# Kernel tuning notes

Hardware: AMD Instinct MI355X
Metric: run time of the kernel (lower is better)

The kernel has to match this reference:

```python
import jax, jax.numpy as jnp
import numpy as np

D = 768      # num_hiddens (hardcoded by dense1/dense2/ln in the source)
H = 12       # num_heads
NEG = -1000000.0
EPS = 1e-5


def setup_inputs() -> dict:
    key = jax.random.key(0)
    ks = jax.random.split(key, 14)
    B, Lq, Lk = 8, 1024, 1024
    s = 0.02
    return {
        "queries": jax.random.normal(ks[0], (B, Lq, D), dtype=jnp.float32),
        "keys":    jax.random.normal(ks[1], (B, Lk, D), dtype=jnp.float32),
        "values":  jax.random.normal(ks[2], (B, Lk, D), dtype=jnp.float32),
        # binary padding masks; count_nonzero along axis 1 gives valid lens
        "mask_1": jax.random.randint(ks[3], (B, Lk), 0, 2, dtype=jnp.int32),
        "mask_2": jax.random.randint(ks[4], (B, Lq), 0, 2, dtype=jnp.int32),
        # projection weights stored as [in, out] (torch Linear is y = x @ W.T)
        "Wq": jax.random.normal(ks[5], (D, D), dtype=jnp.float32) * s,
        "Wk": jax.random.normal(ks[6], (D, D), dtype=jnp.float32) * s,
        "Wv": jax.random.normal(ks[7], (D, D), dtype=jnp.float32) * s,
        "Wo": jax.random.normal(ks[8], (D, D), dtype=jnp.float32) * s,
        "d1_w": jax.random.normal(ks[9], (D, D), dtype=jnp.float32) * s,
        "d1_b": jnp.zeros((D,), dtype=jnp.float32),
        "d2_w": jax.random.normal(ks[10], (D, D), dtype=jnp.float32) * s,
        "d2_b": jnp.zeros((D,), dtype=jnp.float32),
        "ln_g": jnp.ones((D,), dtype=jnp.float32),
        "ln_b": jnp.zeros((D,), dtype=jnp.float32),
    }


def _cross_att(queries, keys, values, mask_1, mask_2,
               Wq, Wk, Wv, Wo, d1_w, d1_b, d2_w, d2_b, ln_g, ln_b):
    B, Lq, _ = queries.shape
    Lk = keys.shape[1]
    hd = D // H
    # project + split heads: [B, H, L, hd]
    q = (queries @ Wq).reshape(B, Lq, H, hd).transpose(0, 2, 1, 3)
    k = (keys    @ Wk).reshape(B, Lk, H, hd).transpose(0, 2, 1, 3)
    v = (values  @ Wv).reshape(B, Lk, H, hd).transpose(0, 2, 1, 3)
    scores = jnp.einsum('bhqd,bhkd->bhqk', q, k) / jnp.sqrt(jnp.float32(hd))
    # dual-axis prefix mask from nonzero counts
    vl1 = jnp.sum(mask_1 != 0, axis=1)  # [B], masks key axis
    vl2 = jnp.sum(mask_2 != 0, axis=1)  # [B], masks query axis
    col_ok = jnp.arange(Lk)[None, None, None, :] < vl1[:, None, None, None]
    row_ok = jnp.arange(Lq)[None, None, :, None] < vl2[:, None, None, None]
    scores = jnp.where(col_ok & row_ok, scores, NEG)
    attn = jax.nn.softmax(scores, axis=-1)
    out = jnp.einsum('bhqk,bhkd->bhqd', attn, v)
    out = out.transpose(0, 2, 1, 3).reshape(B, Lq, D)
    mha = out @ Wo
    ffn = jax.nn.relu(mha @ d1_w + d1_b) @ d2_w + d2_b
    x = ffn + mha  # dropout is identity in eval
    mu = jnp.mean(x, axis=-1, keepdims=True)
    var = jnp.mean(jnp.square(x - mu), axis=-1, keepdims=True)
    return (x - mu) / jnp.sqrt(var + EPS) * ln_g + ln_b


def reference(queries, keys, values, mask_1, mask_2,
              Wq, Wk, Wv, Wo, d1_w, d1_b, d2_w, d2_b, ln_g, ln_b):
    return _cross_att(queries, keys, values, mask_1, mask_2,
                      Wq, Wk, Wv, Wo, d1_w, d1_b, d2_w, d2_b, ln_g, ln_b)
```

## Files before the change

kernel.cpp:

```cpp
#include <hip/hip_runtime.h>
#include <hip/hip_bf16.h>
#include <type_traits>

#define DM   768
#define NH   12
#define HD   64
#define BATCH 8
#define SEQ  1024
#define NROWS (BATCH * SEQ)

typedef short bf16x8 __attribute__((ext_vector_type(8)));
typedef float f32x4 __attribute__((ext_vector_type(4)));

__device__ inline unsigned short f2b(float x) {
    union { float f; unsigned int u; } v; v.f = x;
    return (unsigned short)((v.u + 0x8000u) >> 16);
}
__device__ inline unsigned int f2b2(float lo, float hi) {
    union { float f; unsigned int u; } a, b; a.f = lo; b.f = hi;
    return __builtin_amdgcn_perm(b.u + 0x8000u, a.u + 0x8000u, 0x07060302u);
}
__device__ inline float b2f(unsigned short u) {
    union { float f; unsigned int x; } v; v.x = ((unsigned int)u) << 16;
    return v.f;
}

__device__ inline void gld16(const unsigned short* g, unsigned short* l) {
    __builtin_amdgcn_global_load_lds(
        (const __attribute__((address_space(1))) unsigned int*)g,
        (__attribute__((address_space(3))) unsigned int*)l, 16, 0, 0);
}

__device__ __forceinline__ void mm2(const unsigned short* __restrict__ A,
                                    const unsigned short* __restrict__ Wt,
                                    int m0, int n0, int t,
                                    unsigned short (*As)[128][32],
                                    unsigned short (*Ws)[128][32],
                                    f32x4 (&acc)[4][4]) {
    const int w = t >> 6, lane = t & 63;
    const int quad = lane >> 4, l16 = lane & 15;
    const int wm = w & 1, wn = w >> 1;
    const int srow = 16 * w + (lane >> 2);
    const int scol = 8 * ((lane & 3) ^ ((lane >> 3) & 3));
    const int swr = (quad ^ ((l16 >> 1) & 3)) * 8;

#pragma unroll
    for (int i = 0; i < 4; ++i)
#pragma unroll
        for (int j = 0; j < 4; ++j) acc[i][j] = (f32x4){0.f, 0.f, 0.f, 0.f};

#pragma unroll
    for (int j = 0; j < 2; ++j) {
        gld16(&A[(size_t)(m0 + srow + 64 * j) * DM + scol], &As[0][16 * w + 64 * j][0]);
        gld16(&Wt[(size_t)(n0 + srow + 64 * j) * DM + scol], &Ws[0][16 * w + 64 * j][0]);
    }
    __syncthreads();

    for (int k0 = 0; k0 < DM; k0 += 32) {
        const int cur = (k0 >> 5) & 1;
        if (k0 + 32 < DM) {
#pragma unroll
            for (int j = 0; j < 2; ++j) {
                gld16(&A[(size_t)(m0 + srow + 64 * j) * DM + k0 + 32 + scol],
                      &As[cur ^ 1][16 * w + 64 * j][0]);
                gld16(&Wt[(size_t)(n0 + srow + 64 * j) * DM + k0 + 32 + scol],
                      &Ws[cur ^ 1][16 * w + 64 * j][0]);
            }
        }
        bf16x8 av[4], bv[4];
#pragma unroll
        for (int i = 0; i < 4; ++i)
            av[i] = *(const bf16x8*)&As[cur][wm * 64 + 16 * i + l16][swr];
#pragma unroll
        for (int i = 0; i < 4; ++i)
            bv[i] = *(const bf16x8*)&Ws[cur][wn * 64 + 16 * i + l16][swr];
#pragma unroll
        for (int i = 0; i < 4; ++i)
#pragma unroll
            for (int j = 0; j < 4; ++j)
                acc[i][j] = __builtin_amdgcn_mfma_f32_16x16x32_bf16(bv[j], av[i], acc[i][j], 0, 0, 0);
        __syncthreads();
    }
}

__global__ __launch_bounds__(256) void prep_kernel(const float* __restrict__ w0,
                                                   const float* __restrict__ w1,
                                                   const float* __restrict__ w2,
                                                   const float* __restrict__ w3,
                                                   const float* __restrict__ w4,
                                                   const float* __restrict__ w5,
                                                   unsigned short* __restrict__ wt,
                                                   unsigned short* __restrict__ wob,
                                                   const float* __restrict__ qin,
                                                   const float* __restrict__ kin,
                                                   const float* __restrict__ vin,
                                                   unsigned short* __restrict__ oq,
                                                   unsigned short* __restrict__ ok,
                                                   unsigned short* __restrict__ ov) {
    const int z = blockIdx.z;
    const int t = threadIdx.x;

    if (z >= 6) {
        const int linear = (z - 6) * 576 + blockIdx.y * 24 + blockIdx.x;
        const int c0 = linear * 4;
        const int g = c0 / 3072;
        const int r = c0 % 3072;
        const float* src = (g == 0) ? qin : (g == 1) ? kin : vin;
        unsigned short* dst = (g == 0) ? oq : (g == 1) ? ok : ov;
        const size_t i = ((size_t)r * 256 + t) * 8;
        float4 f[8];
#pragma unroll
        for (int c = 0; c < 4; ++c) {
            f[2 * c]     = ((const float4*)(src + i + (size_t)c * 2048))[0];
            f[2 * c + 1] = ((const float4*)(src + i + (size_t)c * 2048))[1];
        }
#pragma unroll
        for (int c = 0; c < 4; ++c) {
            uint4 p;
            p.x = f2b2(f[2 * c].x, f[2 * c].y);
            p.y = f2b2(f[2 * c].z, f[2 * c].w);
            p.z = f2b2(f[2 * c + 1].x, f[2 * c + 1].y);
            p.w = f2b2(f[2 * c + 1].z, f[2 * c + 1].w);
            *(uint4*)(dst + i + (size_t)c * 2048) = p;
        }
        return;
    }

    {
        __shared__ float tile[32][33];
        const float* W = (z == 0) ? w0 : (z == 1) ? w1 : (z == 2) ? w2
                       : (z == 3) ? w3 : (z == 4) ? w4 : w5;
        unsigned short* Wt = wt + (size_t)z * DM * DM;
        const int n0 = blockIdx.x * 32;
        const int k0 = blockIdx.y * 32;
        const int tx = t & 31;
        const int ty = t >> 5;
        float v[4];
#pragma unroll
        for (int r = 0; r < 4; ++r) {
            v[r] = W[(size_t)(k0 + ty + 8 * r) * DM + n0 + tx];
            tile[ty + 8 * r][tx] = v[r];
        }
        if (z == 3) {
#pragma unroll
            for (int r = 0; r < 4; ++r)
                wob[(size_t)(k0 + ty + 8 * r) * DM + n0 + tx] = f2b(v[r]);
        }
        __syncthreads();
#pragma unroll
        for (int r = 0; r < 4; ++r)
            Wt[(size_t)(n0 + ty + 8 * r) * DM + k0 + tx] = f2b(tile[tx][ty + 8 * r]);
    }
}

__global__ __launch_bounds__(256) void qkv_gemm(const unsigned short* __restrict__ aq,
                                                const unsigned short* __restrict__ akk,
                                                const unsigned short* __restrict__ av_,
                                                unsigned short* __restrict__ wt,
                                                const unsigned short* __restrict__ wob,
                                                unsigned short* __restrict__ c0,
                                                unsigned short* __restrict__ c1,
                                                unsigned short* __restrict__ c2,
                                                const int* __restrict__ m1,
                                                const int* __restrict__ m2,
                                                int* __restrict__ lens) {
    __shared__ __align__(16) unsigned short As[2][128][32];
    __shared__ __align__(16) unsigned short Ws[2][128][32];

    const int t = threadIdx.x;
    const size_t WT = (size_t)DM * DM;

    const unsigned short* A;
    const unsigned short* Wop;
    unsigned short* C;
    float cs = 1.0f;
    int m0, n0;

    if (blockIdx.y == 0) {
        if (blockIdx.x >= 52) return;
        if (blockIdx.x >= 36) {
            const int bid = blockIdx.x - 36;
            int* redi = (int*)&As[0][0][0];
            const int b = bid & 7;
            const int* m = (bid < 8) ? m1 : m2;
            int cnt = 0;
            for (int i = t; i < SEQ; i += 256) cnt += (m[b * SEQ + i] != 0) ? 1 : 0;
            redi[t] = cnt;
            __syncthreads();
            for (int off = 128; off > 0; off >>= 1) {
                if (t < off) redi[t] += redi[t + off];
                __syncthreads();
            }
            if (t == 0) lens[bid] = redi[0];
            return;
        }
        A = wt + 4 * WT;
        Wop = wob;
        C = wt + 6 * WT;
        m0 = (blockIdx.x % 6) * 128;
        n0 = (blockIdx.x / 6) * 128;
    } else {
        const int yy = blockIdx.y - 1;
        const int g = yy / 6;
        m0 = blockIdx.x * 128;
        n0 = (yy % 6) * 128;
        A = (g == 0) ? aq : (g == 1) ? akk : av_;
        Wop = wt + (size_t)g * WT;
        C = (g == 0) ? c0 : (g == 1) ? c1 : c2;
        cs = (g == 0) ? 0.18033688f : 1.0f;
    }

    f32x4 acc[4][4];
    mm2(A, Wop, m0, n0, t, As, Ws, acc);

    const int w = t >> 6, lane = t & 63;
    const int quad = lane >> 4, l16 = lane & 15;
    const int wm = w & 1, wn = w >> 1;

#pragma unroll
    for (int i = 0; i < 4; ++i) {
        const int tok = m0 + wm * 64 + 16 * i + l16;
        unsigned short* crow = &C[(size_t)tok * DM + n0 + wn * 64 + quad * 4];
#pragma unroll
        for (int j = 0; j < 4; ++j) {
            uint2 pr;
            pr.x = f2b2(acc[i][j][0] * cs, acc[i][j][1] * cs);
            pr.y = f2b2(acc[i][j][2] * cs, acc[i][j][3] * cs);
            *(uint2*)(crow + 16 * j) = pr;
        }
    }
}

__global__ __launch_bounds__(256) void vpart_kernel(const unsigned short* __restrict__ v,
                                                    float* __restrict__ vp) {
    __shared__ float red[4][64];
    const int t = threadIdx.x;
    const int bh = blockIdx.x;
    const int chunk = blockIdx.y;
    const int b = bh / NH, h = bh % NH;
    const int d = t & 63, rg = t >> 6;
    const unsigned short* base =
        v + (size_t)(b * SEQ + chunk * 128 + rg * 32) * DM + h * HD + d;
    float s = 0.0f;
#pragma unroll 4
    for (int i = 0; i < 32; ++i) s += b2f(base[(size_t)i * DM]);
    red[rg][d] = s;
    __syncthreads();
    if (rg == 0)
        vp[((size_t)bh * 8 + chunk) * 64 + d] = red[0][d] + red[1][d] + red[2][d] + red[3][d];
}

template <typename CT>
__global__ __launch_bounds__(256) void gemm_bf(const unsigned short* __restrict__ A,
                                               const unsigned short* __restrict__ Wt,
                                               CT* __restrict__ C,
                                               const float* __restrict__ bias,
                                               const unsigned short* __restrict__ res,
                                               int relu) {
    __shared__ __align__(16) unsigned short As[2][128][32];
    __shared__ __align__(16) unsigned short Ws[2][128][32];

    const int t = threadIdx.x;
    const int m0 = blockIdx.x * 128;
    const int n0 = blockIdx.y * 128;

    f32x4 acc[4][4];
    mm2(A, Wt, m0, n0, t, As, Ws, acc);

    const int w = t >> 6, lane = t & 63;
    const int quad = lane >> 4, l16 = lane & 15;
    const int wm = w & 1, wn = w >> 1;

#pragma unroll
    for (int i = 0; i < 4; ++i) {
        const int tok = m0 + wm * 64 + 16 * i + l16;
#pragma unroll
        for (int j = 0; j < 4; ++j) {
            const int fb = n0 + wn * 64 + 16 * j + quad * 4;
            float cv0 = acc[i][j][0], cv1 = acc[i][j][1];
            float cv2 = acc[i][j][2], cv3 = acc[i][j][3];
            if (bias) {
                const float4 bb = *(const float4*)&bias[fb];
                cv0 += bb.x; cv1 += bb.y; cv2 += bb.z; cv3 += bb.w;
            }
            if (relu) {
                cv0 = fmaxf(cv0, 0.0f); cv1 = fmaxf(cv1, 0.0f);
                cv2 = fmaxf(cv2, 0.0f); cv3 = fmaxf(cv3, 0.0f);
            }
            if (res) {
                const uint2 rr = *(const uint2*)&res[(size_t)tok * DM + fb];
                cv0 += b2f((unsigned short)(rr.x & 0xffffu));
                cv1 += b2f((unsigned short)(rr.x >> 16));
                cv2 += b2f((unsigned short)(rr.y & 0xffffu));
                cv3 += b2f((unsigned short)(rr.y >> 16));
            }
            if constexpr (std::is_same<CT, float>::value) {
                float4 o4; o4.x = cv0; o4.y = cv1; o4.z = cv2; o4.w = cv3;
                *(float4*)&C[(size_t)tok * DM + fb] = o4;
            } else {
                uint2 pr;
                pr.x = f2b2(cv0, cv1);
                pr.y = f2b2(cv2, cv3);
                *(uint2*)&C[(size_t)tok * DM + fb] = pr;
            }
        }
    }
}

__global__ __launch_bounds__(256) void gemm_mh(const unsigned short* __restrict__ A,
                                               const unsigned short* __restrict__ wt,
                                               unsigned short* __restrict__ cm,
                                               unsigned short* __restrict__ ch,
                                               const float* __restrict__ d1b) {
    __shared__ __align__(16) unsigned short As[2][128][32];
    __shared__ __align__(16) unsigned short Ws[2][128][32];

    const int t = threadIdx.x;
    const int unit = blockIdx.y / 6;
    const unsigned short* Wt = wt + (size_t)(unit ? 6 : 3) * DM * DM;
    unsigned short* C = unit ? ch : cm;
    const int m0 = blockIdx.x * 128;
    const int n0 = (blockIdx.y % 6) * 128;

    f32x4 acc[4][4];
    mm2(A, Wt, m0, n0, t, As, Ws, acc);

    const int w = t >> 6, lane = t & 63;
    const int quad = lane >> 4, l16 = lane & 15;
    const int wm = w & 1, wn = w >> 1;

#pragma unroll
    for (int i = 0; i < 4; ++i) {
        const int tok = m0 + wm * 64 + 16 * i + l16;
#pragma unroll
        for (int j = 0; j < 4; ++j) {
            const int fb = n0 + wn * 64 + 16 * j + quad * 4;
            float cv0 = acc[i][j][0], cv1 = acc[i][j][1];
            float cv2 = acc[i][j][2], cv3 = acc[i][j][3];
            if (unit) {
                const float4 bb = *(const float4*)&d1b[fb];
                cv0 = fmaxf(cv0 + bb.x, 0.0f);
                cv1 = fmaxf(cv1 + bb.y, 0.0f);
                cv2 = fmaxf(cv2 + bb.z, 0.0f);
                cv3 = fmaxf(cv3 + bb.w, 0.0f);
            }
            uint2 pr;
            pr.x = f2b2(cv0, cv1);
            pr.y = f2b2(cv2, cv3);
            *(uint2*)&C[(size_t)tok * DM + fb] = pr;
        }
    }
}

__global__ __launch_bounds__(256) void attn_mfma(const unsigned short* Q,
                                                 const unsigned short* __restrict__ K,
                                                 const unsigned short* __restrict__ V,
                                                 unsigned short* O,
                                                 const int* __restrict__ lens,
                                                 const float* __restrict__ vp) {
    __shared__ __align__(16) unsigned short Ks[64][72];
    __shared__ __align__(16) unsigned short Vt[64][72];
    __shared__ __align__(16) unsigned short Ps[4][16][72];

    const int t = threadIdx.x;
    const int bid = blockIdx.x;
    const int q0 = (bid & 15) * 64;
    const int h = (bid >> 4) % NH;
    const int b = bid / (16 * NH);
    const int vl1 = lens[b];
    const int vl2 = lens[8 + b];
    const int wid = t >> 6;
    const int lane = t & 63;
    const int quad = lane >> 4;
    const int l16 = lane & 15;
    const size_t vpb = (size_t)(b * NH + h) * 8 * 64;

    if (q0 >= vl2 || vl1 == 0) {
        float vm[4];
#pragma unroll
        for (int ct = 0; ct < 4; ++ct) {
            float s = 0.0f;
#pragma unroll
            for (int c = 0; c < 8; ++c) s += vp[vpb + (size_t)c * 64 + 16 * ct + l16];
            vm[ct] = s * (1.0f / 1024.0f);
        }
#pragma unroll
        for (int r = 0; r < 4; ++r) {
            const size_t row = (size_t)(b * SEQ + q0 + 16 * wid + quad * 4 + r);
#pragma unroll
            for (int ct = 0; ct < 4; ++ct)
                O[row * DM + h * HD + 16 * ct + l16] = f2b(vm[ct]);
        }
        return;
    }

    bf16x8 qa0, qa1;
    {
        const unsigned short* qp =
            &Q[(size_t)(b * SEQ + q0 + 16 * wid + l16) * DM + h * HD + quad * 8];
        qa0 = *(const bf16x8*)qp;
        qa1 = *(const bf16x8*)(qp + 32);
    }

    f32x4 o[4];
#pragma unroll
    for (int ct = 0; ct < 4; ++ct) o[ct] = (f32x4){0.f, 0.f, 0.f, 0.f};
    float suml[4];
    bool rbad[4];
#pragma unroll
    for (int r = 0; r < 4; ++r) {
        suml[r] = 0.0f;
        rbad[r] = (q0 + 16 * wid + quad * 4 + r) >= vl2;
    }

    const int nt = (vl1 + 63) >> 6;

    const int kkr = t >> 3;
    const int khc = (t & 7) * 8;
    const unsigned short* kbase = &K[(size_t)(b * SEQ) * DM + h * HD];
    const unsigned short* vbase = &V[(size_t)(b * SEQ) * DM + h * HD];

    uint4 kr0 = *(const uint4*)&kbase[(size_t)kkr * DM + khc];
    uint4 kr1 = *(const uint4*)&kbase[(size_t)(kkr + 32) * DM + khc];
    uint4 vr0 = *(const uint4*)&vbase[(size_t)lane * DM + wid * 16];
    uint4 vr1 = *(const uint4*)&vbase[(size_t)lane * DM + wid * 16 + 8];

    const int k2 = l16 >> 2;

    for (int tile = 0; tile < nt; ++tile) {
        const int c0 = tile * 64;
        *(uint4*)&Ks[kkr][khc] = kr0;
        *(uint4*)&Ks[kkr + 32][khc] = kr1;
        {
            union { uint4 u; unsigned short s[8]; } va, vb;
            va.u = vr0; vb.u = vr1;
#pragma unroll
            for (int j = 0; j < 8; ++j) Vt[wid * 16 + j][lane] = va.s[j];
#pragma unroll
            for (int j = 0; j < 8; ++j) Vt[wid * 16 + 8 + j][lane] = vb.s[j];
        }
        __syncthreads();

        if (tile < nt - 1) {
            const int c1 = c0 + 64;
            kr0 = *(const uint4*)&kbase[(size_t)(c1 + kkr) * DM + khc];
            kr1 = *(const uint4*)&kbase[(size_t)(c1 + kkr + 32) * DM + khc];
            vr0 = *(const uint4*)&vbase[(size_t)(c1 + lane) * DM + wid * 16];
            vr1 = *(const uint4*)&vbase[(size_t)(c1 + lane) * DM + wid * 16 + 8];
        }

        f32x4 s[4];
#pragma unroll
        for (int ct = 0; ct < 4; ++ct) {
            f32x4 acc = (f32x4){0.f, 0.f, 0.f, 0.f};
            bf16x8 b0v = *(const bf16x8*)&Ks[16 * ct + l16][quad * 8];
            bf16x8 b1v = *(const bf16x8*)&Ks[16 * ct + l16][32 + quad * 8];
            acc = __builtin_amdgcn_mfma_f32_16x16x32_bf16(qa0, b0v, acc, 0, 0, 0);
            acc = __builtin_amdgcn_mfma_f32_16x16x32_bf16(qa1, b1v, acc, 0, 0, 0);
            s[ct] = acc;
        }
#pragma unroll
        for (int ct = 0; ct < 4; ++ct) {
            const bool kok = (c0 + 16 * ct + l16) < vl1;
#pragma unroll
            for (int r = 0; r < 4; ++r) {
                float e = __builtin_amdgcn_exp2f(s[ct][r]);
                float p = kok ? e : 0.0f;
                s[ct][r] = p;
                suml[r] += p;
            }
        }
#pragma unroll
        for (int ct = 0; ct < 4; ++ct) {
            const int gidx = 2 * ct + (l16 >> 3);
            const int c = l16 & 7;
            const int gs = (gidx ^ quad) * 8 + c;
#pragma unroll
            for (int r = 0; r < 4; ++r)
                Ps[wid][quad * 4 + r][gs] = f2b(s[ct][r]);
        }
        bf16x8 pa0 = *(const bf16x8*)&Ps[wid][l16][(quad ^ k2) * 8];
        bf16x8 pa1 = *(const bf16x8*)&Ps[wid][l16][((4 + quad) ^ k2) * 8];
#pragma unroll
        for (int ct = 0; ct < 4; ++ct) {
            bf16x8 vb0 = *(const bf16x8*)&Vt[16 * ct + l16][quad * 8];
            bf16x8 vb1 = *(const bf16x8*)&Vt[16 * ct + l16][32 + quad * 8];
            o[ct] = __builtin_amdgcn_mfma_f32_16x16x32_bf16(pa0, vb0, o[ct], 0, 0, 0);
            o[ct] = __builtin_amdgcn_mfma_f32_16x16x32_bf16(pa1, vb1, o[ct], 0, 0, 0);
        }
        __syncthreads();
    }

#pragma unroll
    for (int d = 1; d < 16; d <<= 1) {
#pragma unroll
        for (int r = 0; r < 4; ++r) suml[r] += __shfl_xor(suml[r], d, 64);
    }

    float vm[4];
    if (rbad[0] || rbad[3]) {
#pragma unroll
        for (int ct = 0; ct < 4; ++ct) {
            float s = 0.0f;
#pragma unroll
            for (int c = 0; c < 8; ++c) s += vp[vpb + (size_t)c * 64 + 16 * ct + l16];
            vm[ct] = s * (1.0f / 1024.0f);
        }
    }
#pragma unroll
    for (int r = 0; r < 4; ++r) {
        const float inv = 1.0f / suml[r];
        const size_t row = (size_t)(b * SEQ + q0 + 16 * wid + quad * 4 + r);
#pragma unroll
        for (int ct = 0; ct < 4; ++ct) {
            const float val = rbad[r] ? vm[ct] : o[ct][r] * inv;
            O[row * DM + h * HD + 16 * ct + l16] = f2b(val);
        }
    }
}

__global__ __launch_bounds__(256) void ln_kernel(float* __restrict__ X,
                                                 const float* __restrict__ g,
                                                 const float* __restrict__ bvec) {
    __shared__ float red[256];
    const int row = blockIdx.x;
    const int t = threadIdx.x;
    float* xr = X + (size_t)row * DM;
    float x0 = xr[t];
    float x1 = xr[t + 256];
    float x2 = xr[t + 512];
    red[t] = x0 + x1 + x2;
    __syncthreads();
    for (int off = 128; off > 0; off >>= 1) {
        if (t < off) red[t] += red[t + off];
        __syncthreads();
    }
    float mu = red[0] * (1.0f / 768.0f);
    __syncthreads();
    float d0 = x0 - mu, d1 = x1 - mu, d2 = x2 - mu;
    red[t] = d0 * d0 + d1 * d1 + d2 * d2;
    __syncthreads();
    for (int off = 128; off > 0; off >>= 1) {
        if (t < off) red[t] += red[t + off];
        __syncthreads();
    }
    float rstd = rsqrtf(red[0] * (1.0f / 768.0f) + 1e-5f);
    xr[t]       = d0 * rstd * g[t]       + bvec[t];
    xr[t + 256] = d1 * rstd * g[t + 256] + bvec[t + 256];
    xr[t + 512] = d2 * rstd * g[t + 512] + bvec[t + 512];
}

extern "C" void kernel_launch(void* const* d_in, const int* in_sizes, int n_in,
                              void* d_out, int out_size, void* d_ws, size_t ws_size,
                              hipStream_t stream) {
    const float* queries = (const float*)d_in[0];
    const float* keys    = (const float*)d_in[1];
    const float* values  = (const float*)d_in[2];
    const int* mask1 = (const int*)d_in[3];
    const int* mask2 = (const int*)d_in[4];
    const float* Wq  = (const float*)d_in[5];
    const float* Wk  = (const float*)d_in[6];
    const float* Wv  = (const float*)d_in[7];
    const float* Wo  = (const float*)d_in[8];
    const float* d1w = (const float*)d_in[9];
    const float* d1b = (const float*)d_in[10];
    const float* d2w = (const float*)d_in[11];
    const float* d2b = (const float*)d_in[12];
    const float* lng = (const float*)d_in[13];
    const float* lnb = (const float*)d_in[14];

    char* ws = (char*)d_ws;
    int* lens = (int*)ws;
    float* vp = (float*)(ws + 256);
    const size_t VP = (size_t)96 * 8 * 64 * sizeof(float);
    const size_t NB = (size_t)NROWS * DM * sizeof(unsigned short);
    const size_t WT = (size_t)DM * DM;
    unsigned short* b0 = (unsigned short*)(ws + 256 + VP);
    unsigned short* b1 = (unsigned short*)(ws + 256 + VP + NB);
    unsigned short* b2 = (unsigned short*)(ws + 256 + VP + 2 * NB);
    unsigned short* wt = (unsigned short*)(ws + 256 + VP + 3 * NB);
    unsigned short* aq = (unsigned short*)(ws + 256 + VP + 3 * NB + 7 * WT * sizeof(unsigned short));
    unsigned short* ak = aq + (size_t)NROWS * DM;
    unsigned short* av = ak + (size_t)NROWS * DM;
    unsigned short* wob = av + (size_t)NROWS * DM;
    float* xout = (float*)d_out;

    prep_kernel<<<dim3(24, 24, 10), 256, 0, stream>>>(Wq, Wk, Wv, Wo, d1w, d2w,
                                                      wt, wob, queries, keys, values,
                                                      aq, ak, av);

    qkv_gemm<<<dim3(64, 19), 256, 0, stream>>>(aq, ak, av, wt, wob, b0, b1, b2,
                                               mask1, mask2, lens);

    vpart_kernel<<<dim3(96, 8), 256, 0, stream>>>(b2, vp);

    attn_mfma<<<16 * NH * BATCH, 256, 0, stream>>>(b0, b1, b2, b0, lens, vp);

    gemm_mh<<<dim3(64, 12), 256, 0, stream>>>(b0, wt, b1, b2, d1b);

    gemm_bf<float><<<dim3(64, 6), 256, 0, stream>>>(b2, wt + 5 * WT, xout, d2b, b1, 0);

    ln_kernel<<<NROWS, 256, 0, stream>>>(xout, lng, lnb);
}
```

Before: 302.0 us.

## Triple-buffer GEMM mainloop and fuse V column sums into QKV epilogue

The shared GEMM mainloop moves from double-buffered LDS staging with a __syncthreads per step to a three-stage ring. It uses explicit vmcnt waits and raw s_barrier, so loads run two tiles ahead of the MFMA work. The V per-chunk column sums, which the separate vpart kernel computed by re-reading V from global memory, are now reduced from the accumulators in the QKV GEMM epilogue using shuffles and LDS, and that kernel launch is dropped. The prep kernel also reorders its grid so the activation-conversion blocks come first. The cost is 50% more LDS per block (24 KB vs 16 KB), which may lower occupancy, and the hand-written vmcnt counts must match the exact number of outstanding loads.

After: 299.2 us. Within noise of the previous version (-0.9%).

```diff
diff --git a/kernel.cpp b/kernel.cpp
--- a/kernel.cpp
+++ b/kernel.cpp
@@ -31,7 +31,7 @@
         (__attribute__((address_space(3))) unsigned int*)l, 16, 0, 0);
 }
 
-__device__ __forceinline__ void mm2(const unsigned short* __restrict__ A,
+__device__ __forceinline__ void mm3(const unsigned short* __restrict__ A,
                                     const unsigned short* __restrict__ Wt,
                                     int m0, int n0, int t,
                                     unsigned short (*As)[128][32],
@@ -49,37 +49,44 @@
 #pragma unroll
         for (int j = 0; j < 4; ++j) acc[i][j] = (f32x4){0.f, 0.f, 0.f, 0.f};
 
-#pragma unroll
-    for (int j = 0; j < 2; ++j) {
-        gld16(&A[(size_t)(m0 + srow + 64 * j) * DM + scol], &As[0][16 * w + 64 * j][0]);
-        gld16(&Wt[(size_t)(n0 + srow + 64 * j) * DM + scol], &Ws[0][16 * w + 64 * j][0]);
-    }
-    __syncthreads();
-
-    for (int k0 = 0; k0 < DM; k0 += 32) {
-        const int cur = (k0 >> 5) & 1;
-        if (k0 + 32 < DM) {
-#pragma unroll
-            for (int j = 0; j < 2; ++j) {
-                gld16(&A[(size_t)(m0 + srow + 64 * j) * DM + k0 + 32 + scol],
-                      &As[cur ^ 1][16 * w + 64 * j][0]);
-                gld16(&Wt[(size_t)(n0 + srow + 64 * j) * DM + k0 + 32 + scol],
-                      &Ws[cur ^ 1][16 * w + 64 * j][0]);
-            }
-        }
+    const unsigned short* aP = &A[(size_t)(m0 + srow) * DM + scol];
+    const unsigned short* wP = &Wt[(size_t)(n0 + srow) * DM + scol];
+
+    auto stage = [&](int kk, int b) {
+#pragma unroll
+        for (int j = 0; j < 2; ++j) {
+            gld16(aP + (size_t)(64 * j) * DM + kk * 32, &As[b][16 * w + 64 * j][0]);
+            gld16(wP + (size_t)(64 * j) * DM + kk * 32, &Ws[b][16 * w + 64 * j][0]);
+        }
+    };
+    auto compute = [&](int b) {
         bf16x8 av[4], bv[4];
 #pragma unroll
         for (int i = 0; i < 4; ++i)
-            av[i] = *(const bf16x8*)&As[cur][wm * 64 + 16 * i + l16][swr];
+            av[i] = *(const bf16x8*)&As[b][wm * 64 + 16 * i + l16][swr];
 #pragma unroll
         for (int i = 0; i < 4; ++i)
-            bv[i] = *(const bf16x8*)&Ws[cur][wn * 64 + 16 * i + l16][swr];
+            bv[i] = *(const bf16x8*)&Ws[b][wn * 64 + 16 * i + l16][swr];
 #pragma unroll
         for (int i = 0; i < 4; ++i)
 #pragma unroll
             for (int j = 0; j < 4; ++j)
                 acc[i][j] = __builtin_amdgcn_mfma_f32_16x16x32_bf16(bv[j], av[i], acc[i][j], 0, 0, 0);
-        __syncthreads();
+    };
+
+    stage(0, 0);
+    stage(1, 1);
+#pragma unroll
+    for (int k = 0; k < 24; ++k) {
+        if (k + 2 < 24) stage(k + 2, (k + 2) % 3);
+        if (k <= 21)      asm volatile("s_waitcnt vmcnt(8)" ::: "memory");
+        else if (k == 22) asm volatile("s_waitcnt vmcnt(4)" ::: "memory");
+        else              asm volatile("s_waitcnt vmcnt(0)" ::: "memory");
+        __builtin_amdgcn_s_barrier();
+        __builtin_amdgcn_sched_barrier(0);
+        compute(k % 3);
+        __builtin_amdgcn_sched_barrier(0);
+        __builtin_amdgcn_s_barrier();
     }
 }
 
@@ -100,8 +107,8 @@
     const int z = blockIdx.z;
     const int t = threadIdx.x;
 
-    if (z >= 6) {
-        const int linear = (z - 6) * 576 + blockIdx.y * 24 + blockIdx.x;
+    if (z < 4) {
+        const int linear = z * 576 + blockIdx.y * 24 + blockIdx.x;
         const int c0 = linear * 4;
         const int g = c0 / 3072;
         const int r = c0 % 3072;
@@ -128,9 +135,10 @@
 
     {
         __shared__ float tile[32][33];
-        const float* W = (z == 0) ? w0 : (z == 1) ? w1 : (z == 2) ? w2
-                       : (z == 3) ? w3 : (z == 4) ? w4 : w5;
-        unsigned short* Wt = wt + (size_t)z * DM * DM;
+        const int zz = z - 4;
+        const float* W = (zz == 0) ? w0 : (zz == 1) ? w1 : (zz == 2) ? w2
+                       : (zz == 3) ? w3 : (zz == 4) ? w4 : w5;
+        unsigned short* Wt = wt + (size_t)zz * DM * DM;
         const int n0 = blockIdx.x * 32;
         const int k0 = blockIdx.y * 32;
         const int tx = t & 31;
@@ -141,7 +149,7 @@
             v[r] = W[(size_t)(k0 + ty + 8 * r) * DM + n0 + tx];
             tile[ty + 8 * r][tx] = v[r];
         }
-        if (z == 3) {
+        if (zz == 3) {
 #pragma unroll
             for (int r = 0; r < 4; ++r)
                 wob[(size_t)(k0 + ty + 8 * r) * DM + n0 + tx] = f2b(v[r]);
@@ -163,9 +171,10 @@
                                                 unsigned short* __restrict__ c2,
                                                 const int* __restrict__ m1,
                                                 const int* __restrict__ m2,
-                                                int* __restrict__ lens) {
-    __shared__ __align__(16) unsigned short As[2][128][32];
-    __shared__ __align__(16) unsigned short Ws[2][128][32];
+                                                int* __restrict__ lens,
+                                                float* __restrict__ vp) {
+    __shared__ __align__(16) unsigned short As[3][128][32];
+    __shared__ __align__(16) unsigned short Ws[3][128][32];
 
     const int t = threadIdx.x;
     const size_t WT = (size_t)DM * DM;
@@ -174,7 +183,7 @@
     const unsigned short* Wop;
     unsigned short* C;
     float cs = 1.0f;
-    int m0, n0;
+    int m0, n0, g = -1;
 
     if (blockIdx.y == 0) {
         if (blockIdx.x >= 52) return;
@@ -201,7 +210,7 @@
         n0 = (blockIdx.x / 6) * 128;
     } else {
         const int yy = blockIdx.y - 1;
-        const int g = yy / 6;
+        g = yy / 6;
         m0 = blockIdx.x * 128;
         n0 = (yy % 6) * 128;
         A = (g == 0) ? aq : (g == 1) ? akk : av_;
@@ -211,7 +220,7 @@
     }
 
     f32x4 acc[4][4];
-    mm2(A, Wop, m0, n0, t, As, Ws, acc);
+    mm3(A, Wop, m0, n0, t, As, Ws, acc);
 
     const int w = t >> 6, lane = t & 63;
     const int quad = lane >> 4, l16 = lane & 15;
@@ -229,25 +238,37 @@
             *(uint2*)(crow + 16 * j) = pr;
         }
     }
-}
-
-__global__ __launch_bounds__(256) void vpart_kernel(const unsigned short* __restrict__ v,
-                                                    float* __restrict__ vp) {
-    __shared__ float red[4][64];
-    const int t = threadIdx.x;
-    const int bh = blockIdx.x;
-    const int chunk = blockIdx.y;
-    const int b = bh / NH, h = bh % NH;
-    const int d = t & 63, rg = t >> 6;
-    const unsigned short* base =
-        v + (size_t)(b * SEQ + chunk * 128 + rg * 32) * DM + h * HD + d;
-    float s = 0.0f;
-#pragma unroll 4
-    for (int i = 0; i < 32; ++i) s += b2f(base[(size_t)i * DM]);
-    red[rg][d] = s;
-    __syncthreads();
-    if (rg == 0)
-        vp[((size_t)bh * 8 + chunk) * 64 + d] = red[0][d] + red[1][d] + red[2][d] + red[3][d];
+
+    if (g == 2) {
+        float s2[4][4];
+#pragma unroll
+        for (int j = 0; j < 4; ++j)
+#pragma unroll
+            for (int r = 0; r < 4; ++r) {
+                float sv = acc[0][j][r] + acc[1][j][r] + acc[2][j][r] + acc[3][j][r];
+#pragma unroll
+                for (int d = 1; d < 16; d <<= 1) sv += __shfl_xor(sv, d, 64);
+                s2[j][r] = sv;
+            }
+        float mine = 0.f;
+#pragma unroll
+        for (int j = 0; j < 4; ++j)
+#pragma unroll
+            for (int r = 0; r < 4; ++r)
+                if ((l16 >> 2) == j && (l16 & 3) == r) mine = s2[j][r];
+        float* sc = (float*)&As[0][0][0];
+        const int slot = (wn * 4 + quad) * 16 + l16;
+        __syncthreads();
+        if (wm == 1) sc[slot] = mine;
+        __syncthreads();
+        if (wm == 0) {
+            const int col = n0 + wn * 64 + 16 * (l16 >> 2) + quad * 4 + (l16 & 3);
+            const int bb = m0 >> 10;
+            const int chunk = (m0 >> 7) & 7;
+            const int hh = col >> 6;
+            vp[((size_t)(bb * NH + hh) * 8 + chunk) * 64 + (col & 63)] = mine + sc[slot];
+        }
+    }
 }
 
 template <typename CT>
@@ -257,15 +278,15 @@
                                                const float* __restrict__ bias,
                                                const unsigned short* __restrict__ res,
                                                int relu) {
-    __shared__ __align__(16) unsigned short As[2][128][32];
-    __shared__ __align__(16) unsigned short Ws[2][128][32];
+    __shared__ __align__(16) unsigned short As[3][128][32];
+    __shared__ __align__(16) unsigned short Ws[3][128][32];
 
     const int t = threadIdx.x;
     const int m0 = blockIdx.x * 128;
     const int n0 = blockIdx.y * 128;
 
     f32x4 acc[4][4];
-    mm2(A, Wt, m0, n0, t, As, Ws, acc);
+    mm3(A, Wt, m0, n0, t, As, Ws, acc);
 
     const int w = t >> 6, lane = t & 63;
     const int quad = lane >> 4, l16 = lane & 15;
@@ -312,8 +333,8 @@
                                                unsigned short* __restrict__ cm,
                                                unsigned short* __restrict__ ch,
                                                const float* __restrict__ d1b) {
-    __shared__ __align__(16) unsigned short As[2][128][32];
-    __shared__ __align__(16) unsigned short Ws[2][128][32];
+    __shared__ __align__(16) unsigned short As[3][128][32];
+    __shared__ __align__(16) unsigned short Ws[3][128][32];
 
     const int t = threadIdx.x;
     const int unit = blockIdx.y / 6;
@@ -323,7 +344,7 @@
     const int n0 = (blockIdx.y % 6) * 128;
 
     f32x4 acc[4][4];
-    mm2(A, Wt, m0, n0, t, As, Ws, acc);
+    mm3(A, Wt, m0, n0, t, As, Ws, acc);
 
     const int w = t >> 6, lane = t & 63;
     const int quad = lane >> 4, l16 = lane & 15;
@@ -590,9 +611,7 @@
                                                       aq, ak, av);
 
     qkv_gemm<<<dim3(64, 19), 256, 0, stream>>>(aq, ak, av, wt, wob, b0, b1, b2,
-                                               mask1, mask2, lens);
-
-    vpart_kernel<<<dim3(96, 8), 256, 0, stream>>>(b2, vp);
+                                               mask1, mask2, lens, vp);
 
     attn_mfma<<<16 * NH * BATCH, 256, 0, stream>>>(b0, b1, b2, b0, lens, vp);
 
```
